# Performance work log

Measured on AMD Instinct MI355X. Metric: run time of the kernel, lower is better.

The kernel has to match this reference:

```python
import jax, jax.numpy as jnp
import numpy as np
import math

B, S, IN, H, M = 4, 2048, 256, 128, 128  # mem_dim must equal hidden_size


def _xavier(key, shape):
    fan_in, fan_out = shape[0], shape[-1]
    lim = math.sqrt(6.0 / (fan_in + fan_out))
    return jax.random.uniform(key, shape, jnp.float32, -lim, lim)


def setup_inputs() -> dict:
    key = jax.random.key(0)
    ks = jax.random.split(key, 8)
    return dict(
        x=jax.random.normal(ks[0], (B, S, IN), jnp.float32),
        c0=jnp.zeros((M, M), jnp.float32),   # init_hidden matrix memory
        n0=jnp.zeros((M, 1), jnp.float32),   # init_hidden normalizer
        w_q=_xavier(ks[1], (IN, H)), b_q=jnp.zeros((H,), jnp.float32),
        w_k=_xavier(ks[2], (IN, M)), b_k=jnp.zeros((M,), jnp.float32),
        w_v=_xavier(ks[3], (IN, M)), b_v=jnp.zeros((M,), jnp.float32),
        w_i=_xavier(ks[4], (IN, 1)), b_i=jnp.zeros((1,), jnp.float32),
        w_f=_xavier(ks[5], (IN, 1)), b_f=jnp.zeros((1,), jnp.float32),
        w_o=_xavier(ks[6], (IN, H)), b_o=jnp.zeros((H,), jnp.float32),
    )


def reference(x, c0, n0, w_q, b_q, w_k, b_k, w_v, b_v, w_i, b_i, w_f, b_f, w_o, b_o):
    Bb, Ss, Ii = x.shape
    Mm = w_k.shape[1]
    Hh = w_q.shape[1]
    xf = x.reshape(Bb * Ss, Ii)                                  # [N, IN]
    q = xf @ w_q + b_q                                           # [N, H]
    k = (xf @ w_k + b_k) * (1.0 / math.sqrt(Mm))                 # [N, M]
    v = xf @ w_v + b_v                                           # [N, M]
    i_t = jnp.exp(xf @ w_i + b_i)                                # [N, 1]
    f_t = jax.nn.sigmoid(xf @ w_f + b_f)                         # [N, 1]
    # Original loop never updates c_prev: c_t[n] = f[n]*c0 + i[n]*outer(v[n], k[n])
    c = f_t[:, :, None] * c0[None] + i_t[:, :, None] * (v[:, :, None] * k[:, None, :])  # [N, M, M]
    n = f_t[:, :, None] * n0[None] + i_t[:, :, None] * k[:, :, None]                    # [N, M, 1]
    c = c.reshape(Bb, Ss, Mm, Mm)
    n = n.reshape(Bb, Ss, Mm, 1)
    q4 = q.reshape(Bb, Ss, Hh)
    nq = jnp.einsum('bsm,bsm->bs', n[..., 0], q4)                # n^T q
    denom = jnp.maximum(jnp.abs(nq), 1.0)[..., None]             # max(|n^T q|, 1)
    h_tilde = jnp.einsum('bsmk,bsk->bsm', c, q4) / denom         # (c_t q) / denom
    o = jax.nn.sigmoid(xf @ w_o + b_o).reshape(Bb, Ss, Hh)
    h = o * h_tilde                                              # [B, S, H]
    return (h, c, n)
```

## Files before the change

kernel.cpp:

```cpp
#include <hip/hip_runtime.h>
#include <math.h>

#define B_    4
#define S_    2048
#define IN_   256
#define H_    128
#define M_    128
#define NROWS (B_ * S_)
#define RPB   16
#define TPB   256
#define XPAD  260

typedef float f4_t __attribute__((ext_vector_type(4)));

__global__ __launch_bounds__(TPB) void xlstm_proj(
    const float* __restrict__ x,
    const float* __restrict__ c0,
    const float* __restrict__ n0,
    const float* __restrict__ w_q, const float* __restrict__ b_q,
    const float* __restrict__ w_k, const float* __restrict__ b_k,
    const float* __restrict__ w_v, const float* __restrict__ b_v,
    const float* __restrict__ w_i, const float* __restrict__ b_i,
    const float* __restrict__ w_f, const float* __restrict__ b_f,
    const float* __restrict__ w_o, const float* __restrict__ b_o,
    float* __restrict__ out_h,
    float* __restrict__ out_n,
    float* __restrict__ kws,
    float* __restrict__ vws,
    float* __restrict__ ifws)
{
    __shared__ float xs[RPB][XPAD];
    __shared__ float qs[RPB][M_];
    __shared__ float ks[RPB][M_];
    __shared__ float vs[RPB][M_];
    __shared__ float os_[RPB][M_];
    __shared__ float c0qs[RPB][M_];
    __shared__ float itf[RPB][2];
    __shared__ float scal[RPB][2];

    const int t    = threadIdx.x;
    const int row0 = blockIdx.x * RPB;

    for (int p4 = t; p4 < RPB * IN_ / 4; p4 += TPB) {
        int p = p4 * 4;
        float4 v = *(const float4*)(x + (size_t)row0 * IN_ + p);
        int r = p >> 8, c = p & 255;
        *(float4*)&xs[r][c] = v;
    }
    __syncthreads();

    const int col   = t & 127;
    const int rbase = (t >> 7) * 8;

    {
        float accq[8], acck[8], accv[8], acco[8];
        #pragma unroll
        for (int r = 0; r < 8; ++r) { accq[r]=0.f; acck[r]=0.f; accv[r]=0.f; acco[r]=0.f; }

        #pragma unroll 2
        for (int k4 = 0; k4 < IN_; k4 += 4) {
            float4 xr[8];
            #pragma unroll
            for (int r = 0; r < 8; ++r) xr[r] = *(const float4*)&xs[rbase + r][k4];

            int wi = k4 * H_ + col;
            float4 wq, wk, wv, wo;
            wq.x = w_q[wi]; wq.y = w_q[wi + H_]; wq.z = w_q[wi + 2*H_]; wq.w = w_q[wi + 3*H_];
            wk.x = w_k[wi]; wk.y = w_k[wi + M_]; wk.z = w_k[wi + 2*M_]; wk.w = w_k[wi + 3*M_];
            wv.x = w_v[wi]; wv.y = w_v[wi + M_]; wv.z = w_v[wi + 2*M_]; wv.w = w_v[wi + 3*M_];
            wo.x = w_o[wi]; wo.y = w_o[wi + H_]; wo.z = w_o[wi + 2*H_]; wo.w = w_o[wi + 3*H_];

            #pragma unroll
            for (int r = 0; r < 8; ++r) {
                accq[r] = fmaf(xr[r].x, wq.x, fmaf(xr[r].y, wq.y, fmaf(xr[r].z, wq.z, fmaf(xr[r].w, wq.w, accq[r]))));
                acck[r] = fmaf(xr[r].x, wk.x, fmaf(xr[r].y, wk.y, fmaf(xr[r].z, wk.z, fmaf(xr[r].w, wk.w, acck[r]))));
                accv[r] = fmaf(xr[r].x, wv.x, fmaf(xr[r].y, wv.y, fmaf(xr[r].z, wv.z, fmaf(xr[r].w, wv.w, accv[r]))));
                acco[r] = fmaf(xr[r].x, wo.x, fmaf(xr[r].y, wo.y, fmaf(xr[r].z, wo.z, fmaf(xr[r].w, wo.w, acco[r]))));
            }
        }

        const float kscale = 0.08838834764831843f;
        #pragma unroll
        for (int r = 0; r < 8; ++r) {
            int row = rbase + r;
            qs[row][col]  = accq[r] + b_q[col];
            ks[row][col]  = (acck[r] + b_k[col]) * kscale;
            vs[row][col]  = accv[r] + b_v[col];
            float oo      = acco[r] + b_o[col];
            os_[row][col] = 1.f / (1.f + __expf(-oo));
        }
    }

    if (t < 32) {
        int r = t & 15;
        const float* w = (t < 16) ? w_i : w_f;
        float acc = 0.f;
        for (int k = 0; k < IN_; ++k) acc = fmaf(xs[r][k], w[k], acc);
        if (t < 16) itf[r][0] = __expf(acc + b_i[0]);
        else        itf[r][1] = 1.f / (1.f + __expf(-(acc + b_f[0])));
    }
    __syncthreads();

    {
        float acc2[8];
        #pragma unroll
        for (int r = 0; r < 8; ++r) acc2[r] = 0.f;
        const float* c0row = c0 + (size_t)col * M_;
        #pragma unroll 2
        for (int j4 = 0; j4 < M_; j4 += 4) {
            float4 w4 = *(const float4*)(c0row + j4);
            #pragma unroll
            for (int r = 0; r < 8; ++r) {
                float4 q4 = *(const float4*)&qs[rbase + r][j4];
                acc2[r] = fmaf(w4.x, q4.x, fmaf(w4.y, q4.y, fmaf(w4.z, q4.z, fmaf(w4.w, q4.w, acc2[r]))));
            }
        }
        #pragma unroll
        for (int r = 0; r < 8; ++r) c0qs[rbase + r][col] = acc2[r];
    }

    if (t < 32) {
        int r = t & 15;
        float acc = 0.f;
        if (t < 16) {
            for (int j = 0; j < M_; ++j) acc = fmaf(ks[r][j], qs[r][j], acc);
            scal[r][0] = acc;
        } else {
            for (int j = 0; j < M_; ++j) acc = fmaf(n0[j], qs[r][j], acc);
            scal[r][1] = acc;
        }
    }
    __syncthreads();

    #pragma unroll
    for (int r = 0; r < 8; ++r) {
        int row = rbase + r;
        size_t grow = (size_t)(row0 + row);
        float iv = itf[row][0], fv = itf[row][1];
        float kv = ks[row][col];
        float nv = fmaf(fv, n0[col], iv * kv);
        out_n[grow * M_ + col] = nv;
        float nq    = fmaf(fv, scal[row][1], iv * scal[row][0]);
        float denom = fmaxf(fabsf(nq), 1.0f);
        float ht = fmaf(fv, c0qs[row][col], iv * vs[row][col] * scal[row][0]) / denom;
        out_h[grow * H_ + col] = os_[row][col] * ht;
        kws[grow * M_ + col] = kv;
        vws[grow * M_ + col] = vs[row][col];
    }
    if (t < 32) {
        int r = t & 15;
        size_t grow = (size_t)(row0 + r);
        if (t < 16) ifws[grow * 2 + 0] = itf[r][0];
        else        ifws[grow * 2 + 1] = itf[r][1];
    }
}

__global__ __launch_bounds__(TPB) void xlstm_cstream(
    const float* __restrict__ c0,
    const float* __restrict__ kws,
    const float* __restrict__ vws,
    const float* __restrict__ ifws,
    float* __restrict__ out_c)
{
    const int t    = threadIdx.x;
    const int row0 = blockIdx.x * RPB;

    __shared__ float vsh[RPB][M_];
    __shared__ float ksh[RPB][M_];
    __shared__ float2 ish[RPB];

    for (int p4 = t; p4 < RPB * M_ / 4; p4 += TPB) {
        int idx = p4 * 4;
        int r = idx >> 7, c = idx & 127;
        *(float4*)&vsh[r][c] = *(const float4*)(vws + (size_t)row0 * M_ + idx);
        *(float4*)&ksh[r][c] = *(const float4*)(kws + (size_t)row0 * M_ + idx);
    }
    if (t < RPB) ish[t] = *(const float2*)(ifws + (size_t)(row0 + t) * 2);
    __syncthreads();

    float ivr[RPB], fvr[RPB];
    #pragma unroll
    for (int r = 0; r < RPB; ++r) { ivr[r] = ish[r].x; fvr[r] = ish[r].y; }

    const int base = t * 4;
    const int j    = base & 127;

    #pragma unroll 2
    for (int ch = 0; ch < 16; ++ch) {
        int p = (ch << 10) + base;
        int m = p >> 7;
        float4 c0v = *(const float4*)(c0 + p);
        #pragma unroll
        for (int r = 0; r < RPB; ++r) {
            float4 k4 = *(const float4*)&ksh[r][j];
            float  s  = ivr[r] * vsh[r][m];
            f4_t o4;
            o4.x = fmaf(fvr[r], c0v.x, s * k4.x);
            o4.y = fmaf(fvr[r], c0v.y, s * k4.y);
            o4.z = fmaf(fvr[r], c0v.z, s * k4.z);
            o4.w = fmaf(fvr[r], c0v.w, s * k4.w);
            __builtin_nontemporal_store(o4,
                (f4_t*)(out_c + (size_t)(row0 + r) * (M_ * M_) + p));
        }
    }
}

extern "C" void kernel_launch(void* const* d_in, const int* in_sizes, int n_in,
                              void* d_out, int out_size, void* d_ws, size_t ws_size,
                              hipStream_t stream) {
    const float* x   = (const float*)d_in[0];
    const float* c0  = (const float*)d_in[1];
    const float* n0  = (const float*)d_in[2];
    const float* w_q = (const float*)d_in[3];  const float* b_q = (const float*)d_in[4];
    const float* w_k = (const float*)d_in[5];  const float* b_k = (const float*)d_in[6];
    const float* w_v = (const float*)d_in[7];  const float* b_v = (const float*)d_in[8];
    const float* w_i = (const float*)d_in[9];  const float* b_i = (const float*)d_in[10];
    const float* w_f = (const float*)d_in[11]; const float* b_f = (const float*)d_in[12];
    const float* w_o = (const float*)d_in[13]; const float* b_o = (const float*)d_in[14];

    float* out   = (float*)d_out;
    float* out_h = out;
    float* out_c = out + (size_t)NROWS * H_;
    float* out_n = out_c + (size_t)NROWS * M_ * M_;

    float* kws  = (float*)d_ws;
    float* vws  = kws + (size_t)NROWS * M_;
    float* ifws = vws + (size_t)NROWS * M_;

    hipLaunchKernelGGL(xlstm_proj, dim3(NROWS / RPB), dim3(TPB), 0, stream,
                       x, c0, n0, w_q, b_q, w_k, b_k, w_v, b_v,
                       w_i, b_i, w_f, b_f, w_o, b_o,
                       out_h, out_n, kws, vws, ifws);

    hipLaunchKernelGGL(xlstm_cstream, dim3(NROWS / RPB), dim3(TPB), 0, stream,
                       c0, kws, vws, ifws, out_c);
}
```

Baseline: 149.7 us.

## Split-K projection GEMM, parallelize gate/scalar dot products, keep k in registers

The projection kernel now has each half of the block reduce over half of the input dimension for all 16 rows and combine the partials through shared memory, instead of each half taking 8 rows over the full K. This halves redundant weight loads per block. The gate and scalar dot products, previously done serially by 32 threads, are spread across all 256 threads with shuffle reductions. c0·q stays in registers rather than a shared buffer, and launch bounds request 3 blocks per CU. The c-stream kernel caches its per-thread k vectors in registers to avoid repeated LDS reads, at the cost of more register pressure.

```diff
diff --git a/kernel.cpp b/kernel.cpp
--- a/kernel.cpp
+++ b/kernel.cpp
@@ -13,7 +13,7 @@
 
 typedef float f4_t __attribute__((ext_vector_type(4)));
 
-__global__ __launch_bounds__(TPB) void xlstm_proj(
+__global__ __launch_bounds__(TPB, 3) void xlstm_proj(
     const float* __restrict__ x,
     const float* __restrict__ c0,
     const float* __restrict__ n0,
@@ -34,7 +34,6 @@
     __shared__ float ks[RPB][M_];
     __shared__ float vs[RPB][M_];
     __shared__ float os_[RPB][M_];
-    __shared__ float c0qs[RPB][M_];
     __shared__ float itf[RPB][2];
     __shared__ float scal[RPB][2];
 
@@ -50,61 +49,83 @@
     __syncthreads();
 
     const int col   = t & 127;
-    const int rbase = (t >> 7) * 8;
+    const int kh    = t >> 7;
+    const int kbase = kh << 7;
+
+    float accq[16], acck[16], accv[16], acco[16];
+    #pragma unroll
+    for (int r = 0; r < 16; ++r) { accq[r]=0.f; acck[r]=0.f; accv[r]=0.f; acco[r]=0.f; }
+
+    #pragma unroll 2
+    for (int k4 = 0; k4 < 128; k4 += 4) {
+        const int wi = (kbase + k4) * H_ + col;
+        float4 wq, wk, wv, wo;
+        wq.x = w_q[wi]; wq.y = w_q[wi + H_]; wq.z = w_q[wi + 2*H_]; wq.w = w_q[wi + 3*H_];
+        wk.x = w_k[wi]; wk.y = w_k[wi + M_]; wk.z = w_k[wi + 2*M_]; wk.w = w_k[wi + 3*M_];
+        wv.x = w_v[wi]; wv.y = w_v[wi + M_]; wv.z = w_v[wi + 2*M_]; wv.w = w_v[wi + 3*M_];
+        wo.x = w_o[wi]; wo.y = w_o[wi + H_]; wo.z = w_o[wi + 2*H_]; wo.w = w_o[wi + 3*H_];
+
+        #pragma unroll
+        for (int r = 0; r < 16; ++r) {
+            float4 xr = *(const float4*)&xs[r][kbase + k4];
+            accq[r] = fmaf(xr.x, wq.x, fmaf(xr.y, wq.y, fmaf(xr.z, wq.z, fmaf(xr.w, wq.w, accq[r]))));
+            acck[r] = fmaf(xr.x, wk.x, fmaf(xr.y, wk.y, fmaf(xr.z, wk.z, fmaf(xr.w, wk.w, acck[r]))));
+            accv[r] = fmaf(xr.x, wv.x, fmaf(xr.y, wv.y, fmaf(xr.z, wv.z, fmaf(xr.w, wv.w, accv[r]))));
+            acco[r] = fmaf(xr.x, wo.x, fmaf(xr.y, wo.y, fmaf(xr.z, wo.z, fmaf(xr.w, wo.w, acco[r]))));
+        }
+    }
+
+    if (kh == 1) {
+        #pragma unroll
+        for (int r = 0; r < 16; ++r) {
+            qs[r][col]  = accq[r];
+            ks[r][col]  = acck[r];
+            vs[r][col]  = accv[r];
+            os_[r][col] = acco[r];
+        }
+    }
+    __syncthreads();
+    if (kh == 0) {
+        const float kscale = 0.08838834764831843f;
+        #pragma unroll
+        for (int r = 0; r < 16; ++r) {
+            float q  = accq[r] + qs[r][col] + b_q[col];
+            float kk = (acck[r] + ks[r][col] + b_k[col]) * kscale;
+            float vv = accv[r] + vs[r][col] + b_v[col];
+            float oo = acco[r] + os_[r][col] + b_o[col];
+            qs[r][col]  = q;
+            ks[r][col]  = kk;
+            vs[r][col]  = vv;
+            os_[r][col] = 1.f / (1.f + __expf(-oo));
+        }
+    }
+    __syncthreads();
 
     {
-        float accq[8], acck[8], accv[8], acco[8];
-        #pragma unroll
-        for (int r = 0; r < 8; ++r) { accq[r]=0.f; acck[r]=0.f; accv[r]=0.f; acco[r]=0.f; }
-
-        #pragma unroll 2
-        for (int k4 = 0; k4 < IN_; k4 += 4) {
-            float4 xr[8];
-            #pragma unroll
-            for (int r = 0; r < 8; ++r) xr[r] = *(const float4*)&xs[rbase + r][k4];
-
-            int wi = k4 * H_ + col;
-            float4 wq, wk, wv, wo;
-            wq.x = w_q[wi]; wq.y = w_q[wi + H_]; wq.z = w_q[wi + 2*H_]; wq.w = w_q[wi + 3*H_];
-            wk.x = w_k[wi]; wk.y = w_k[wi + M_]; wk.z = w_k[wi + 2*M_]; wk.w = w_k[wi + 3*M_];
-            wv.x = w_v[wi]; wv.y = w_v[wi + M_]; wv.z = w_v[wi + 2*M_]; wv.w = w_v[wi + 3*M_];
-            wo.x = w_o[wi]; wo.y = w_o[wi + H_]; wo.z = w_o[wi + 2*H_]; wo.w = w_o[wi + 3*H_];
-
-            #pragma unroll
-            for (int r = 0; r < 8; ++r) {
-                accq[r] = fmaf(xr[r].x, wq.x, fmaf(xr[r].y, wq.y, fmaf(xr[r].z, wq.z, fmaf(xr[r].w, wq.w, accq[r]))));
-                acck[r] = fmaf(xr[r].x, wk.x, fmaf(xr[r].y, wk.y, fmaf(xr[r].z, wk.z, fmaf(xr[r].w, wk.w, acck[r]))));
-                accv[r] = fmaf(xr[r].x, wv.x, fmaf(xr[r].y, wv.y, fmaf(xr[r].z, wv.z, fmaf(xr[r].w, wv.w, accv[r]))));
-                acco[r] = fmaf(xr[r].x, wo.x, fmaf(xr[r].y, wo.y, fmaf(xr[r].z, wo.z, fmaf(xr[r].w, wo.w, acco[r]))));
-            }
-        }
-
-        const float kscale = 0.08838834764831843f;
-        #pragma unroll
-        for (int r = 0; r < 8; ++r) {
-            int row = rbase + r;
-            qs[row][col]  = accq[r] + b_q[col];
-            ks[row][col]  = (acck[r] + b_k[col]) * kscale;
-            vs[row][col]  = accv[r] + b_v[col];
-            float oo      = acco[r] + b_o[col];
-            os_[row][col] = 1.f / (1.f + __expf(-oo));
-        }
-    }
-
-    if (t < 32) {
-        int r = t & 15;
-        const float* w = (t < 16) ? w_i : w_f;
-        float acc = 0.f;
-        for (int k = 0; k < IN_; ++k) acc = fmaf(xs[r][k], w[k], acc);
-        if (t < 16) itf[r][0] = __expf(acc + b_i[0]);
-        else        itf[r][1] = 1.f / (1.f + __expf(-(acc + b_f[0])));
-    }
-    __syncthreads();
-
+        const int gr = t >> 4, gseg = t & 15;
+        const float* xrow = &xs[gr][gseg * 16];
+        float pi = 0.f, pf = 0.f;
+        #pragma unroll
+        for (int u = 0; u < 4; ++u) {
+            float4 xv  = *(const float4*)(xrow + u * 4);
+            float4 wiv = *(const float4*)(w_i + gseg * 16 + u * 4);
+            float4 wfv = *(const float4*)(w_f + gseg * 16 + u * 4);
+            pi = fmaf(xv.x, wiv.x, fmaf(xv.y, wiv.y, fmaf(xv.z, wiv.z, fmaf(xv.w, wiv.w, pi))));
+            pf = fmaf(xv.x, wfv.x, fmaf(xv.y, wfv.y, fmaf(xv.z, wfv.z, fmaf(xv.w, wfv.w, pf))));
+        }
+        #pragma unroll
+        for (int m = 1; m < 16; m <<= 1) { pi += __shfl_xor(pi, m); pf += __shfl_xor(pf, m); }
+        if (gseg == 0) {
+            itf[gr][0] = __expf(pi + b_i[0]);
+            itf[gr][1] = 1.f / (1.f + __expf(-(pf + b_f[0])));
+        }
+    }
+
+    const int rbase = kh * 8;
+    float c0qr[8];
     {
-        float acc2[8];
-        #pragma unroll
-        for (int r = 0; r < 8; ++r) acc2[r] = 0.f;
+        #pragma unroll
+        for (int r = 0; r < 8; ++r) c0qr[r] = 0.f;
         const float* c0row = c0 + (size_t)col * M_;
         #pragma unroll 2
         for (int j4 = 0; j4 < M_; j4 += 4) {
@@ -112,23 +133,26 @@
             #pragma unroll
             for (int r = 0; r < 8; ++r) {
                 float4 q4 = *(const float4*)&qs[rbase + r][j4];
-                acc2[r] = fmaf(w4.x, q4.x, fmaf(w4.y, q4.y, fmaf(w4.z, q4.z, fmaf(w4.w, q4.w, acc2[r]))));
+                c0qr[r] = fmaf(w4.x, q4.x, fmaf(w4.y, q4.y, fmaf(w4.z, q4.z, fmaf(w4.w, q4.w, c0qr[r]))));
             }
         }
-        #pragma unroll
-        for (int r = 0; r < 8; ++r) c0qs[rbase + r][col] = acc2[r];
-    }
-
-    if (t < 32) {
-        int r = t & 15;
-        float acc = 0.f;
-        if (t < 16) {
-            for (int j = 0; j < M_; ++j) acc = fmaf(ks[r][j], qs[r][j], acc);
-            scal[r][0] = acc;
-        } else {
-            for (int j = 0; j < M_; ++j) acc = fmaf(n0[j], qs[r][j], acc);
-            scal[r][1] = acc;
-        }
+    }
+
+    {
+        const int gr = t >> 4, gseg = t & 15;
+        const int j0 = gseg * 8;
+        float pkq = 0.f, pnq = 0.f;
+        #pragma unroll
+        for (int u = 0; u < 2; ++u) {
+            float4 kk = *(const float4*)&ks[gr][j0 + u * 4];
+            float4 qq = *(const float4*)&qs[gr][j0 + u * 4];
+            float4 nn = *(const float4*)(n0 + j0 + u * 4);
+            pkq = fmaf(kk.x, qq.x, fmaf(kk.y, qq.y, fmaf(kk.z, qq.z, fmaf(kk.w, qq.w, pkq))));
+            pnq = fmaf(nn.x, qq.x, fmaf(nn.y, qq.y, fmaf(nn.z, qq.z, fmaf(nn.w, qq.w, pnq))));
+        }
+        #pragma unroll
+        for (int m = 1; m < 16; m <<= 1) { pkq += __shfl_xor(pkq, m); pnq += __shfl_xor(pnq, m); }
+        if (gseg == 0) { scal[gr][0] = pkq; scal[gr][1] = pnq; }
     }
     __syncthreads();
 
@@ -138,11 +162,10 @@
         size_t grow = (size_t)(row0 + row);
         float iv = itf[row][0], fv = itf[row][1];
         float kv = ks[row][col];
-        float nv = fmaf(fv, n0[col], iv * kv);
-        out_n[grow * M_ + col] = nv;
+        out_n[grow * M_ + col] = fmaf(fv, n0[col], iv * kv);
         float nq    = fmaf(fv, scal[row][1], iv * scal[row][0]);
         float denom = fmaxf(fabsf(nq), 1.0f);
-        float ht = fmaf(fv, c0qs[row][col], iv * vs[row][col] * scal[row][0]) / denom;
+        float ht = fmaf(fv, c0qr[r], iv * vs[row][col] * scal[row][0]) / denom;
         out_h[grow * H_ + col] = os_[row][col] * ht;
         kws[grow * M_ + col] = kv;
         vws[grow * M_ + col] = vs[row][col];
@@ -178,12 +201,16 @@
     if (t < RPB) ish[t] = *(const float2*)(ifws + (size_t)(row0 + t) * 2);
     __syncthreads();
 
-    float ivr[RPB], fvr[RPB];
-    #pragma unroll
-    for (int r = 0; r < RPB; ++r) { ivr[r] = ish[r].x; fvr[r] = ish[r].y; }
-
     const int base = t * 4;
     const int j    = base & 127;
+
+    float ivr[RPB], fvr[RPB];
+    float4 kreg[RPB];
+    #pragma unroll
+    for (int r = 0; r < RPB; ++r) {
+        ivr[r] = ish[r].x; fvr[r] = ish[r].y;
+        kreg[r] = *(const float4*)&ksh[r][j];
+    }
 
     #pragma unroll 2
     for (int ch = 0; ch < 16; ++ch) {
@@ -192,13 +219,12 @@
         float4 c0v = *(const float4*)(c0 + p);
         #pragma unroll
         for (int r = 0; r < RPB; ++r) {
-            float4 k4 = *(const float4*)&ksh[r][j];
-            float  s  = ivr[r] * vsh[r][m];
+            float s = ivr[r] * vsh[r][m];
             f4_t o4;
-            o4.x = fmaf(fvr[r], c0v.x, s * k4.x);
-            o4.y = fmaf(fvr[r], c0v.y, s * k4.y);
-            o4.z = fmaf(fvr[r], c0v.z, s * k4.z);
-            o4.w = fmaf(fvr[r], c0v.w, s * k4.w);
+            o4.x = fmaf(fvr[r], c0v.x, s * kreg[r].x);
+            o4.y = fmaf(fvr[r], c0v.y, s * kreg[r].y);
+            o4.z = fmaf(fvr[r], c0v.z, s * kreg[r].z);
+            o4.w = fmaf(fvr[r], c0v.w, s * kreg[r].w);
             __builtin_nontemporal_store(o4,
                 (f4_t*)(out_c + (size_t)(row0 + r) * (M_ * M_) + p));
         }
```

After: 156.5 us. 4.5% more time.
